# Kernel optimization log

Measured on AMD Instinct MI355X. Metric: run time of the kernel, lower is better.

The kernel has to match this reference:

```python
import jax, jax.numpy as jnp
import numpy as np

B, L, C, H = 32, 512, 512, 8
DH = C // H
LN_EPS = 1e-5


def setup_inputs() -> dict:
    key = jax.random.key(0)
    ks = jax.random.split(key, 5)
    x = jax.random.normal(ks[0], (B, L, C), dtype=jnp.float32)
    # nn.Linear weights are (out, in); y = x @ W.T
    wq = jax.random.normal(ks[1], (C, C), dtype=jnp.float32) * 0.02
    wk = jax.random.normal(ks[2], (C, C), dtype=jnp.float32) * 0.02
    wv = jax.random.normal(ks[3], (C, C), dtype=jnp.float32) * 0.02
    # source zero-inits the bias table; use small randoms so it actually contributes
    bias_table = jax.random.normal(ks[4], (2 * L - 1, H), dtype=jnp.float32) * 0.02
    gamma = jnp.ones((C,), dtype=jnp.float32)
    beta = jnp.zeros((C,), dtype=jnp.float32)
    coords = np.arange(L)
    rel_index = jnp.asarray(coords[None, :] - coords[:, None] + (L - 1), dtype=jnp.int32)  # (L, L)
    return {"x": x, "wq": wq, "wk": wk, "wv": wv, "bias_table": bias_table,
            "gamma": gamma, "beta": beta, "rel_index": rel_index}


def reference(x, wq, wk, wv, bias_table, gamma, beta, rel_index):
    Bx, Lx, Cx = x.shape
    scale = Cx ** (-0.5)  # note: scale uses full emb_size, as in source
    q = (x @ wq.T).reshape(Bx, Lx, H, DH).transpose(0, 2, 1, 3)  # (B,H,L,Dh)
    k = (x @ wk.T).reshape(Bx, Lx, H, DH).transpose(0, 2, 1, 3)
    v = (x @ wv.T).reshape(Bx, Lx, H, DH).transpose(0, 2, 1, 3)
    attn = jax.nn.softmax(jnp.einsum('bhqd,bhkd->bhqk', q, k) * scale, axis=-1)
    # post-softmax relative bias gather-add
    rel_bias = bias_table[rel_index]                # (L, L, H)
    attn = attn + rel_bias.transpose(2, 0, 1)[None]  # (1,H,L,L) broadcast
    out = jnp.einsum('bhqk,bhkd->bhqd', attn, v)
    out = out.transpose(0, 2, 1, 3).reshape(Bx, Lx, Cx)
    mu = out.mean(axis=-1, keepdims=True)
    var = jnp.mean(jnp.square(out - mu), axis=-1, keepdims=True)
    return gamma * (out - mu) * jax.lax.rsqrt(var + LN_EPS) + beta
```

## Files before the change

kernel.cpp:

```cpp
#include <hip/hip_runtime.h>
#include <hip/hip_bf16.h>

typedef unsigned short u16;
typedef __attribute__((ext_vector_type(8))) __bf16 bf16x8;
typedef __attribute__((ext_vector_type(4))) float f32x4;
typedef __attribute__((ext_vector_type(4))) unsigned int u32x4;

#define BB 32
#define LL 512
#define CC 512
#define HH 8
#define DH 64
#define MROWS (BB * LL)
#define NQKV  (3 * CC)

#define XB_BYTES ((size_t)MROWS * CC * 2)
#define WC_BYTES ((size_t)NQKV * CC * 2)
#define QKV_OFF  (XB_BYTES + WC_BYTES)

#define SCALE2 (0.044194173824159216f * 1.4426950408889634f)

#if __has_builtin(__builtin_amdgcn_exp2f)
#define EXP2(x) __builtin_amdgcn_exp2f(x)
#else
#define EXP2(x) exp2f(x)
#endif
#if __has_builtin(__builtin_amdgcn_rcpf)
#define RCP(x) __builtin_amdgcn_rcpf(x)
#else
#define RCP(x) (1.0f / (x))
#endif

__device__ inline u16 f2b(float f) {
  union { float f; unsigned u; } a; a.f = f;
  unsigned u = a.u;
  return (u16)((u + 0x7FFFu + ((u >> 16) & 1u)) >> 16);
}

__device__ inline unsigned pack2(float a, float b) {
  float2 f; f.x = a; f.y = b;
  union { __hip_bfloat162 h; unsigned u; } c;
  c.h = __float22bfloat162_rn(f);
  return c.u;
}

__global__ __launch_bounds__(256) void cvt_x(const float* __restrict__ x, u16* __restrict__ xb) {
  int i = blockIdx.x * 256 + threadIdx.x;
  float4 v = ((const float4*)x)[i];
  uint2 o; o.x = pack2(v.x, v.y); o.y = pack2(v.z, v.w);
  ((uint2*)xb)[i] = o;
}

__global__ __launch_bounds__(256) void cvt_w(const float* __restrict__ wq, const float* __restrict__ wk,
                                             const float* __restrict__ wv, u16* __restrict__ wcat) {
  int i = blockIdx.x * 256 + threadIdx.x;
  int e = i * 4;
  int n = e >> 9;
  int k = e & 511;
  const float* src = (n < 512) ? (wq + (size_t)n * 512)
                   : (n < 1024) ? (wk + (size_t)(n - 512) * 512)
                                : (wv + (size_t)(n - 1024) * 512);
  const float sc = (n < 512) ? SCALE2 : 1.0f;
  float4 v = *(const float4*)(src + k);
  uint2 o; o.x = pack2(v.x * sc, v.y * sc); o.y = pack2(v.z * sc, v.w * sc);
  *(uint2*)(wcat + (size_t)n * 512 + k) = o;
}

typedef __attribute__((address_space(1))) void* as1_void_p;
typedef __attribute__((address_space(3))) void* as3_void_p;

__device__ inline void async16(const u16* g, u16* l) {
#if __has_builtin(__builtin_amdgcn_global_load_lds)
  __builtin_amdgcn_global_load_lds((as1_void_p)g, (as3_void_p)l, 16, 0, 0);
#else
  *(uint4*)l = *(const uint4*)g;
#endif
}

__global__ __launch_bounds__(256) void gemm_qkv(const u16* __restrict__ A, const u16* __restrict__ Bw,
                                                u16* __restrict__ Cm) {
  __shared__ u16 a_lds[128 * 32];
  __shared__ u16 b_lds[128 * 32];
  const int n0 = blockIdx.x * 128, m0 = blockIdx.y * 128;
  const int t = threadIdx.x, l = t & 63;
  const int wrow = ((t >> 7) & 1) * 64, wcol = ((t >> 6) & 1) * 64;
  const int lr = l & 15, lq = l >> 4;

  f32x4 acc[4][4] = {};

  for (int k0 = 0; k0 < 512; k0 += 32) {
    {
      int c0 = t, c1 = t + 256;
      async16(A  + (size_t)(m0 + (c0 >> 2)) * 512 + k0 + (c0 & 3) * 8, &a_lds[c0 * 8]);
      async16(A  + (size_t)(m0 + (c1 >> 2)) * 512 + k0 + (c1 & 3) * 8, &a_lds[c1 * 8]);
      async16(Bw + (size_t)(n0 + (c0 >> 2)) * 512 + k0 + (c0 & 3) * 8, &b_lds[c0 * 8]);
      async16(Bw + (size_t)(n0 + (c1 >> 2)) * 512 + k0 + (c1 & 3) * 8, &b_lds[c1 * 8]);
    }
    __syncthreads();
    bf16x8 af[4], bfr[4];
#pragma unroll
    for (int r = 0; r < 4; ++r) af[r]  = *(const bf16x8*)&a_lds[(wrow + r * 16 + lr) * 32 + lq * 8];
#pragma unroll
    for (int c = 0; c < 4; ++c) bfr[c] = *(const bf16x8*)&b_lds[(wcol + c * 16 + lr) * 32 + lq * 8];
#pragma unroll
    for (int r = 0; r < 4; ++r)
#pragma unroll
      for (int c = 0; c < 4; ++c)
        acc[r][c] = __builtin_amdgcn_mfma_f32_16x16x32_bf16(af[r], bfr[c], acc[r][c], 0, 0, 0);
    __syncthreads();
  }
#pragma unroll
  for (int r = 0; r < 4; ++r) {
#pragma unroll
    for (int i = 0; i < 4; ++i) {
      int m = m0 + wrow + r * 16 + lq * 4 + i;
      u16* crow = Cm + (size_t)m * NQKV + n0 + wcol;
#pragma unroll
      for (int c = 0; c < 4; ++c)
        crow[c * 16 + lr] = f2b(acc[r][c][i]);
    }
  }
}

__global__ __launch_bounds__(256) void transpose_v(const u16* __restrict__ qkv, u16* __restrict__ vT,
                                                   const float* __restrict__ bias_table,
                                                   float* __restrict__ biasT) {
  if (blockIdx.y == 4) {
    if (blockIdx.x < 32) {
      int i = blockIdx.x * 256 + threadIdx.x;
      if (i < 1023 * 8) {
        float v = bias_table[i];
        int rel = i >> 3, hh = i & 7;
        biasT[hh * 1024 + rel] = v;
      }
    }
    return;
  }
  const int bh = blockIdx.x;
  const int b = bh >> 3, h = bh & 7;
  const int lc0 = blockIdx.y * 128;
  __shared__ u16 tile[32 * 72];
  const int t = threadIdx.x;
  for (int lc = lc0; lc < lc0 + 128; lc += 32) {
    int lrow = t >> 3, dcol = (t & 7) * 8;
    const u16* src = qkv + (size_t)(b * 512 + lc + lrow) * NQKV + 1024 + h * 64 + dcol;
    *(uint4*)&tile[lrow * 72 + dcol] = *(const uint4*)src;
    __syncthreads();
    int d = t >> 2, lp = (t & 3) * 8;
    union { ushort4 v4[2]; u16 s[8]; } tmp;
#pragma unroll
    for (int j = 0; j < 8; ++j) tmp.s[j] = tile[(lp + j) * 72 + d];
    *(uint4*)&vT[(size_t)(bh * 64 + d) * 512 + lc + lp] = *(uint4*)&tmp;
    __syncthreads();
  }
}

__global__ __launch_bounds__(256, 4) void attn_kernel(const u16* __restrict__ qkv, const u16* __restrict__ vT,
                                                      const float* __restrict__ biasT,
                                                      float* __restrict__ out) {
  __shared__ u16 p_lds[32 * 512];
  __shared__ float bias_lds[544];
  __shared__ float reds[4][32];

  const int flat = blockIdx.x;
  const int bh = ((flat >> 7) << 3) | (flat & 7);
  const int q0 = ((flat >> 3) & 15) * 32;
  const int b = bh >> 3, h = bh & 7;
  const int t = threadIdx.x, l = t & 63, w = t >> 6;
  const int lr = l & 15, lq = l >> 4;

  {
    const int rel0 = 480 - q0;
    const float* bsrc = biasT + h * 1024 + rel0;
    for (int i = t; i < 543; i += 256)
      bias_lds[i] = bsrc[i];
  }
  asm volatile("s_waitcnt vmcnt(0)" ::: "memory");

  bf16x8 bq[2][2];
#pragma unroll
  for (int qt = 0; qt < 2; ++qt) {
    const u16* qrow = qkv + (size_t)(b * 512 + q0 + qt * 16 + lr) * NQKV + h * 64;
    bq[qt][0] = *(const bf16x8*)(qrow + lq * 8);
    bq[qt][1] = *(const bf16x8*)(qrow + 32 + lq * 8);
  }

  const u16* kbase = qkv + (size_t)(b * 512 + w * 128 + lr) * NQKV + 512 + h * 64 + lq * 8;
  u32x4 akr[4][2];
  f32x4 sT[2][8];

#define KISSUE(slot, ct) { const u16* kr = kbase + (size_t)(ct) * 16 * NQKV;   \
    asm volatile("global_load_dwordx4 %0, %2, off\n\t"                         \
                 "global_load_dwordx4 %1, %2, off offset:64"                   \
                 : "=&v"(akr[slot][0]), "=&v"(akr[slot][1]) : "v"(kr)); }
#define KSTEP(ct, lit, doissue) {                                              \
    if (doissue) KISSUE(((ct) + 3) & 3, (ct) + 3)                              \
    asm volatile("s_waitcnt vmcnt(" lit ")"                                    \
                 : "+v"(akr[(ct) & 3][0]), "+v"(akr[(ct) & 3][1]));            \
    bf16x8 ak0 = __builtin_bit_cast(bf16x8, akr[(ct) & 3][0]);                 \
    bf16x8 ak1 = __builtin_bit_cast(bf16x8, akr[(ct) & 3][1]);                 \
    f32x4 a0 = {0.f, 0.f, 0.f, 0.f}, a1 = {0.f, 0.f, 0.f, 0.f};                \
    a0 = __builtin_amdgcn_mfma_f32_16x16x32_bf16(ak0, bq[0][0], a0, 0, 0, 0);  \
    a0 = __builtin_amdgcn_mfma_f32_16x16x32_bf16(ak1, bq[0][1], a0, 0, 0, 0);  \
    a1 = __builtin_amdgcn_mfma_f32_16x16x32_bf16(ak0, bq[1][0], a1, 0, 0, 0);  \
    a1 = __builtin_amdgcn_mfma_f32_16x16x32_bf16(ak1, bq[1][1], a1, 0, 0, 0);  \
    sT[0][ct] = a0; sT[1][ct] = a1; }

  KISSUE(0, 0) KISSUE(1, 1) KISSUE(2, 2)
  KSTEP(0, "6", 1) KSTEP(1, "6", 1) KSTEP(2, "6", 1) KSTEP(3, "6", 1)
  KSTEP(4, "6", 1) KSTEP(5, "4", 0) KSTEP(6, "2", 0) KSTEP(7, "0", 0)
#undef KSTEP
#undef KISSUE

  float sq[2];
#pragma unroll
  for (int qt = 0; qt < 2; ++qt) {
    float s0 = 0.f, s1 = 0.f, s2 = 0.f, s3 = 0.f;
#pragma unroll
    for (int ct = 0; ct < 8; ++ct) {
      float e0 = EXP2(sT[qt][ct][0]);
      float e1 = EXP2(sT[qt][ct][1]);
      float e2 = EXP2(sT[qt][ct][2]);
      float e3 = EXP2(sT[qt][ct][3]);
      sT[qt][ct][0] = e0; sT[qt][ct][1] = e1;
      sT[qt][ct][2] = e2; sT[qt][ct][3] = e3;
      s0 += e0; s1 += e1; s2 += e2; s3 += e3;
    }
    sq[qt] = (s0 + s1) + (s2 + s3);
  }
  {
    float t0 = sq[0], t1 = sq[1];
    float u0 = __shfl_xor(t0, 16, 64), u1 = __shfl_xor(t1, 16, 64);
    t0 += u0; t1 += u1;
    u0 = __shfl_xor(t0, 32, 64); u1 = __shfl_xor(t1, 32, 64);
    sq[0] = t0 + u0; sq[1] = t1 + u1;
  }
  if (lq == 0) { reds[w][lr] = sq[0]; reds[w][16 + lr] = sq[1]; }

  asm volatile("s_waitcnt lgkmcnt(0)" ::: "memory");
  __builtin_amdgcn_s_barrier();
  asm volatile("" ::: "memory");

  float rinv[2];
#pragma unroll
  for (int qt = 0; qt < 2; ++qt)
    rinv[qt] = RCP(reds[0][qt * 16 + lr] + reds[1][qt * 16 + lr] +
                   reds[2][qt * 16 + lr] + reds[3][qt * 16 + lr]);

  const u16* vrow = vT + (size_t)(bh * 64 + w * 16 + lr) * 512 + lq * 8;
  u32x4 avr[8];
#define VISSUE(slot, olit)                                                     \
  asm volatile("global_load_dwordx4 %0, %1, off offset:" olit                  \
               : "=&v"(avr[slot]) : "v"(vrow));
  VISSUE(0, "0")   VISSUE(1, "64")  VISSUE(2, "128") VISSUE(3, "192")
  VISSUE(4, "256") VISSUE(5, "320") VISSUE(6, "384") VISSUE(7, "448")

#define PACK_QT(qt)                                                            \
  {                                                                            \
    const int qlocal = (qt) * 16 + lr;                                         \
    u16* prow = p_lds + qlocal * 512;                                          \
    const int boff = w * 128 + lq * 4 + 31 - qlocal;                           \
    _Pragma("unroll")                                                          \
    for (int ct = 0; ct < 8; ++ct) {                                           \
      const int gsw = w * 8 + (ct ^ (lr & 7));                                 \
      float p0 = sT[qt][ct][0] * rinv[qt] + bias_lds[boff + ct * 16 + 0];      \
      float p1 = sT[qt][ct][1] * rinv[qt] + bias_lds[boff + ct * 16 + 1];      \
      float p2 = sT[qt][ct][2] * rinv[qt] + bias_lds[boff + ct * 16 + 2];      \
      float p3 = sT[qt][ct][3] * rinv[qt] + bias_lds[boff + ct * 16 + 3];      \
      uint2 pk; pk.x = pack2(p0, p1); pk.y = pack2(p2, p3);                    \
      *(uint2*)&prow[gsw * 16 + lq * 4] = pk;                                  \
    }                                                                          \
  }
  PACK_QT(0)
  PACK_QT(1)
#undef PACK_QT

  asm volatile("s_waitcnt lgkmcnt(0)" ::: "memory");
  __builtin_amdgcn_s_barrier();
  asm volatile("" ::: "memory");

  f32x4 accP[2] = {};
  bf16x8 bp[2][2];
#define LDP(kb, qt) \
  (*(const bf16x8*)&p_lds[((qt) * 16 + lr) * 512 + \
    (((2 * (kb) + (lq >> 1)) & ~7) | (((2 * (kb) + (lq >> 1)) & 7) ^ (lr & 7))) * 16 + (lq & 1) * 8])
  bp[0][0] = LDP(0, 0);
  bp[0][1] = LDP(0, 1);
#define PVSTEP(kb, lit, doissue, olit) {                                       \
    asm volatile("s_waitcnt vmcnt(" lit ")" : "+v"(avr[(kb) & 7]));            \
    if ((kb) < 15) {                                                           \
      bp[((kb) + 1) & 1][0] = LDP((kb) + 1, 0);                                \
      bp[((kb) + 1) & 1][1] = LDP((kb) + 1, 1);                                \
    }                                                                          \
    bf16x8 av = __builtin_bit_cast(bf16x8, avr[(kb) & 7]);                     \
    accP[0] = __builtin_amdgcn_mfma_f32_16x16x32_bf16(av, bp[(kb) & 1][0], accP[0], 0, 0, 0); \
    accP[1] = __builtin_amdgcn_mfma_f32_16x16x32_bf16(av, bp[(kb) & 1][1], accP[1], 0, 0, 0); \
    if (doissue) VISSUE((kb) & 7, olit) }
  PVSTEP(0,  "7", 1, "512") PVSTEP(1,  "7", 1, "576")
  PVSTEP(2,  "7", 1, "640") PVSTEP(3,  "7", 1, "704")
  PVSTEP(4,  "7", 1, "768") PVSTEP(5,  "7", 1, "832")
  PVSTEP(6,  "7", 1, "896") PVSTEP(7,  "7", 1, "960")
  PVSTEP(8,  "7", 0, "0")   PVSTEP(9,  "6", 0, "0")
  PVSTEP(10, "5", 0, "0")   PVSTEP(11, "4", 0, "0")
  PVSTEP(12, "3", 0, "0")   PVSTEP(13, "2", 0, "0")
  PVSTEP(14, "1", 0, "0")   PVSTEP(15, "0", 0, "0")
#undef PVSTEP
#undef VISSUE
#undef LDP
#pragma unroll
  for (int qt = 0; qt < 2; ++qt)
    *(f32x4*)&out[(size_t)(b * 512 + q0 + qt * 16 + lr) * 512 + h * 64 + w * 16 + lq * 4] = accP[qt];
}

__global__ __launch_bounds__(256) void ln_kernel(float* __restrict__ out,
                                                 const float* __restrict__ gamma,
                                                 const float* __restrict__ beta) {
  const int t = threadIdx.x;
  const int r2 = t >> 7;
  const int row = blockIdx.x * 2 + r2;
  const int c = (t & 127) * 4;
  float* p = out + (size_t)row * 512;
  float4 v = *(float4*)(p + c);
  float s = v.x + v.y + v.z + v.w;
  float s2 = v.x * v.x + v.y * v.y + v.z * v.z + v.w * v.w;
#pragma unroll
  for (int d = 1; d < 64; d <<= 1) { s += __shfl_xor(s, d, 64); s2 += __shfl_xor(s2, d, 64); }
  __shared__ float ps[4], ps2[4];
  const int wv = t >> 6;
  if ((t & 63) == 0) { ps[wv] = s; ps2[wv] = s2; }
  __syncthreads();
  s  = ps[r2 * 2]  + ps[r2 * 2 + 1];
  s2 = ps2[r2 * 2] + ps2[r2 * 2 + 1];
  float mu = s * (1.0f / 512.0f);
  float var = s2 * (1.0f / 512.0f) - mu * mu;
  float rs = rsqrtf(var + 1e-5f);
  float4 g = *(const float4*)(gamma + c);
  float4 bb = *(const float4*)(beta + c);
  v.x = g.x * (v.x - mu) * rs + bb.x;
  v.y = g.y * (v.y - mu) * rs + bb.y;
  v.z = g.z * (v.z - mu) * rs + bb.z;
  v.w = g.w * (v.w - mu) * rs + bb.w;
  *(float4*)(p + c) = v;
}

extern "C" void kernel_launch(void* const* d_in, const int* in_sizes, int n_in,
                              void* d_out, int out_size, void* d_ws, size_t ws_size,
                              hipStream_t stream) {
  const float* x    = (const float*)d_in[0];
  const float* wq   = (const float*)d_in[1];
  const float* wk   = (const float*)d_in[2];
  const float* wv   = (const float*)d_in[3];
  const float* bias = (const float*)d_in[4];
  const float* gamma = (const float*)d_in[5];
  const float* beta  = (const float*)d_in[6];
  float* out = (float*)d_out;

  char* ws = (char*)d_ws;
  u16* xb   = (u16*)ws;
  u16* wcat = (u16*)(ws + XB_BYTES);
  u16* qkv  = (u16*)(ws + QKV_OFF);
  u16* vT   = xb;
  float* biasT = (float*)(ws + XB_BYTES);

  cvt_x<<<dim3((MROWS * CC) / 4 / 256), 256, 0, stream>>>(x, xb);
  cvt_w<<<dim3((NQKV * CC) / 4 / 256), 256, 0, stream>>>(wq, wk, wv, wcat);
  gemm_qkv<<<dim3(NQKV / 128, MROWS / 128), 256, 0, stream>>>(xb, wcat, qkv);
  transpose_v<<<dim3(256, 5), 256, 0, stream>>>(qkv, vT, bias, biasT);
  attn_kernel<<<dim3(16 * 256), 256, 0, stream>>>(qkv, vT, biasT, out);
  ln_kernel<<<dim3(MROWS / 2), 256, 0, stream>>>(out, gamma, beta);
}
```

Measured before the change: 224.3 us.

## Process four 32-row query tiles per attention block in a loop

Each attention block now loops over four consecutive 32-row query tiles, covering 128 query rows, and the grid shrinks from 4096 to 1024 blocks. The relative-bias slice is loaded into LDS once per block with a wider window, and the reduction buffer is double-buffered so consecutive iterations do not collide. The aim is to amortize per-block setup (bias load, launch, address calculation) over more work. In exchange, iterations within a block run serially, there are fewer blocks to hide latency across CUs, and K/V are still re-read for every tile.

```diff
diff --git a/kernel.cpp b/kernel.cpp
--- a/kernel.cpp
+++ b/kernel.cpp
@@ -159,35 +159,47 @@
                                                       const float* __restrict__ biasT,
                                                       float* __restrict__ out) {
   __shared__ u16 p_lds[32 * 512];
-  __shared__ float bias_lds[544];
-  __shared__ float reds[4][32];
+  __shared__ float bias_lds[640];
+  __shared__ float reds[2][4][32];
 
   const int flat = blockIdx.x;
-  const int bh = ((flat >> 7) << 3) | (flat & 7);
-  const int q0 = ((flat >> 3) & 15) * 32;
-  const int b = bh >> 3, h = bh & 7;
+  const int h = flat & 7;
+  const int qslot = (flat >> 3) & 3;
+  const int b = flat >> 5;
+  const int bh = b * 8 + h;
+  const int q0 = qslot * 128;
   const int t = threadIdx.x, l = t & 63, w = t >> 6;
   const int lr = l & 15, lq = l >> 4;
 
   {
-    const int rel0 = 480 - q0;
+    const int rel0 = 384 - q0;
     const float* bsrc = biasT + h * 1024 + rel0;
-    for (int i = t; i < 543; i += 256)
+    for (int i = t; i < 639; i += 256)
       bias_lds[i] = bsrc[i];
   }
   asm volatile("s_waitcnt vmcnt(0)" ::: "memory");
 
-  bf16x8 bq[2][2];
-#pragma unroll
-  for (int qt = 0; qt < 2; ++qt) {
-    const u16* qrow = qkv + (size_t)(b * 512 + q0 + qt * 16 + lr) * NQKV + h * 64;
-    bq[qt][0] = *(const bf16x8*)(qrow + lq * 8);
-    bq[qt][1] = *(const bf16x8*)(qrow + 32 + lq * 8);
-  }
-
   const u16* kbase = qkv + (size_t)(b * 512 + w * 128 + lr) * NQKV + 512 + h * 64 + lq * 8;
-  u32x4 akr[4][2];
-  f32x4 sT[2][8];
+  const u16* vrow  = vT  + (size_t)(bh * 64 + w * 16 + lr) * 512 + lq * 8;
+
+#pragma unroll 1
+  for (int j = 0; j < 4; ++j) {
+    const int q0j = q0 + j * 32;
+
+    u32x4 bqr[2][2];
+    {
+      const u16* q0r = qkv + (size_t)(b * 512 + q0j + lr) * NQKV + h * 64 + lq * 8;
+      const u16* q1r = q0r + (size_t)16 * NQKV;
+      asm volatile("global_load_dwordx4 %0, %2, off\n\t"
+                   "global_load_dwordx4 %1, %2, off offset:64"
+                   : "=&v"(bqr[0][0]), "=&v"(bqr[0][1]) : "v"(q0r));
+      asm volatile("global_load_dwordx4 %0, %2, off\n\t"
+                   "global_load_dwordx4 %1, %2, off offset:64"
+                   : "=&v"(bqr[1][0]), "=&v"(bqr[1][1]) : "v"(q1r));
+    }
+
+    u32x4 akr[4][2];
+    f32x4 sT[2][8];
 
 #define KISSUE(slot, ct) { const u16* kr = kbase + (size_t)(ct) * 16 * NQKV;   \
     asm volatile("global_load_dwordx4 %0, %2, off\n\t"                         \
@@ -200,92 +212,94 @@
     bf16x8 ak0 = __builtin_bit_cast(bf16x8, akr[(ct) & 3][0]);                 \
     bf16x8 ak1 = __builtin_bit_cast(bf16x8, akr[(ct) & 3][1]);                 \
     f32x4 a0 = {0.f, 0.f, 0.f, 0.f}, a1 = {0.f, 0.f, 0.f, 0.f};                \
-    a0 = __builtin_amdgcn_mfma_f32_16x16x32_bf16(ak0, bq[0][0], a0, 0, 0, 0);  \
-    a0 = __builtin_amdgcn_mfma_f32_16x16x32_bf16(ak1, bq[0][1], a0, 0, 0, 0);  \
-    a1 = __builtin_amdgcn_mfma_f32_16x16x32_bf16(ak0, bq[1][0], a1, 0, 0, 0);  \
-    a1 = __builtin_amdgcn_mfma_f32_16x16x32_bf16(ak1, bq[1][1], a1, 0, 0, 0);  \
+    a0 = __builtin_amdgcn_mfma_f32_16x16x32_bf16(ak0, __builtin_bit_cast(bf16x8, bqr[0][0]), a0, 0, 0, 0); \
+    a0 = __builtin_amdgcn_mfma_f32_16x16x32_bf16(ak1, __builtin_bit_cast(bf16x8, bqr[0][1]), a0, 0, 0, 0); \
+    a1 = __builtin_amdgcn_mfma_f32_16x16x32_bf16(ak0, __builtin_bit_cast(bf16x8, bqr[1][0]), a1, 0, 0, 0); \
+    a1 = __builtin_amdgcn_mfma_f32_16x16x32_bf16(ak1, __builtin_bit_cast(bf16x8, bqr[1][1]), a1, 0, 0, 0); \
     sT[0][ct] = a0; sT[1][ct] = a1; }
 
-  KISSUE(0, 0) KISSUE(1, 1) KISSUE(2, 2)
-  KSTEP(0, "6", 1) KSTEP(1, "6", 1) KSTEP(2, "6", 1) KSTEP(3, "6", 1)
-  KSTEP(4, "6", 1) KSTEP(5, "4", 0) KSTEP(6, "2", 0) KSTEP(7, "0", 0)
+    KISSUE(0, 0) KISSUE(1, 1) KISSUE(2, 2)
+    asm volatile("s_waitcnt vmcnt(6)"
+                 : "+v"(bqr[0][0]), "+v"(bqr[0][1]), "+v"(bqr[1][0]), "+v"(bqr[1][1]));
+    KSTEP(0, "6", 1) KSTEP(1, "6", 1) KSTEP(2, "6", 1) KSTEP(3, "6", 1)
+    KSTEP(4, "6", 1) KSTEP(5, "4", 0) KSTEP(6, "2", 0) KSTEP(7, "0", 0)
 #undef KSTEP
 #undef KISSUE
 
-  float sq[2];
-#pragma unroll
-  for (int qt = 0; qt < 2; ++qt) {
-    float s0 = 0.f, s1 = 0.f, s2 = 0.f, s3 = 0.f;
-#pragma unroll
-    for (int ct = 0; ct < 8; ++ct) {
-      float e0 = EXP2(sT[qt][ct][0]);
-      float e1 = EXP2(sT[qt][ct][1]);
-      float e2 = EXP2(sT[qt][ct][2]);
-      float e3 = EXP2(sT[qt][ct][3]);
-      sT[qt][ct][0] = e0; sT[qt][ct][1] = e1;
-      sT[qt][ct][2] = e2; sT[qt][ct][3] = e3;
-      s0 += e0; s1 += e1; s2 += e2; s3 += e3;
-    }
-    sq[qt] = (s0 + s1) + (s2 + s3);
-  }
-  {
-    float t0 = sq[0], t1 = sq[1];
-    float u0 = __shfl_xor(t0, 16, 64), u1 = __shfl_xor(t1, 16, 64);
-    t0 += u0; t1 += u1;
-    u0 = __shfl_xor(t0, 32, 64); u1 = __shfl_xor(t1, 32, 64);
-    sq[0] = t0 + u0; sq[1] = t1 + u1;
-  }
-  if (lq == 0) { reds[w][lr] = sq[0]; reds[w][16 + lr] = sq[1]; }
-
-  asm volatile("s_waitcnt lgkmcnt(0)" ::: "memory");
-  __builtin_amdgcn_s_barrier();
-  asm volatile("" ::: "memory");
-
-  float rinv[2];
-#pragma unroll
-  for (int qt = 0; qt < 2; ++qt)
-    rinv[qt] = RCP(reds[0][qt * 16 + lr] + reds[1][qt * 16 + lr] +
-                   reds[2][qt * 16 + lr] + reds[3][qt * 16 + lr]);
-
-  const u16* vrow = vT + (size_t)(bh * 64 + w * 16 + lr) * 512 + lq * 8;
-  u32x4 avr[8];
+    float sq[2];
+#pragma unroll
+    for (int qt = 0; qt < 2; ++qt) {
+      float s0 = 0.f, s1 = 0.f, s2 = 0.f, s3 = 0.f;
+#pragma unroll
+      for (int ct = 0; ct < 8; ++ct) {
+        float e0 = EXP2(sT[qt][ct][0]);
+        float e1 = EXP2(sT[qt][ct][1]);
+        float e2 = EXP2(sT[qt][ct][2]);
+        float e3 = EXP2(sT[qt][ct][3]);
+        sT[qt][ct][0] = e0; sT[qt][ct][1] = e1;
+        sT[qt][ct][2] = e2; sT[qt][ct][3] = e3;
+        s0 += e0; s1 += e1; s2 += e2; s3 += e3;
+      }
+      sq[qt] = (s0 + s1) + (s2 + s3);
+    }
+    {
+      float t0 = sq[0], t1 = sq[1];
+      float u0 = __shfl_xor(t0, 16, 64), u1 = __shfl_xor(t1, 16, 64);
+      t0 += u0; t1 += u1;
+      u0 = __shfl_xor(t0, 32, 64); u1 = __shfl_xor(t1, 32, 64);
+      sq[0] = t0 + u0; sq[1] = t1 + u1;
+    }
+    float (*rd)[32] = reds[j & 1];
+    if (lq == 0) { rd[w][lr] = sq[0]; rd[w][16 + lr] = sq[1]; }
+
+    asm volatile("s_waitcnt lgkmcnt(0)" ::: "memory");
+    __builtin_amdgcn_s_barrier();
+    asm volatile("" ::: "memory");
+
+    float rinv[2];
+#pragma unroll
+    for (int qt = 0; qt < 2; ++qt)
+      rinv[qt] = RCP(rd[0][qt * 16 + lr] + rd[1][qt * 16 + lr] +
+                     rd[2][qt * 16 + lr] + rd[3][qt * 16 + lr]);
+
+    u32x4 avr[8];
 #define VISSUE(slot, olit)                                                     \
-  asm volatile("global_load_dwordx4 %0, %1, off offset:" olit                  \
-               : "=&v"(avr[slot]) : "v"(vrow));
-  VISSUE(0, "0")   VISSUE(1, "64")  VISSUE(2, "128") VISSUE(3, "192")
-  VISSUE(4, "256") VISSUE(5, "320") VISSUE(6, "384") VISSUE(7, "448")
+    asm volatile("global_load_dwordx4 %0, %1, off offset:" olit                \
+                 : "=&v"(avr[slot]) : "v"(vrow));
+    VISSUE(0, "0")   VISSUE(1, "64")  VISSUE(2, "128") VISSUE(3, "192")
+    VISSUE(4, "256") VISSUE(5, "320") VISSUE(6, "384") VISSUE(7, "448")
 
 #define PACK_QT(qt)                                                            \
-  {                                                                            \
-    const int qlocal = (qt) * 16 + lr;                                         \
-    u16* prow = p_lds + qlocal * 512;                                          \
-    const int boff = w * 128 + lq * 4 + 31 - qlocal;                           \
-    _Pragma("unroll")                                                          \
-    for (int ct = 0; ct < 8; ++ct) {                                           \
-      const int gsw = w * 8 + (ct ^ (lr & 7));                                 \
-      float p0 = sT[qt][ct][0] * rinv[qt] + bias_lds[boff + ct * 16 + 0];      \
-      float p1 = sT[qt][ct][1] * rinv[qt] + bias_lds[boff + ct * 16 + 1];      \
-      float p2 = sT[qt][ct][2] * rinv[qt] + bias_lds[boff + ct * 16 + 2];      \
-      float p3 = sT[qt][ct][3] * rinv[qt] + bias_lds[boff + ct * 16 + 3];      \
-      uint2 pk; pk.x = pack2(p0, p1); pk.y = pack2(p2, p3);                    \
-      *(uint2*)&prow[gsw * 16 + lq * 4] = pk;                                  \
-    }                                                                          \
-  }
-  PACK_QT(0)
-  PACK_QT(1)
+    {                                                                          \
+      const int qlocal = (qt) * 16 + lr;                                       \
+      u16* prow = p_lds + qlocal * 512;                                        \
+      const int boff = w * 128 + lq * 4 + 127 - 32 * j - qlocal;               \
+      _Pragma("unroll")                                                        \
+      for (int ct = 0; ct < 8; ++ct) {                                         \
+        const int gsw = w * 8 + (ct ^ (lr & 7));                               \
+        float p0 = sT[qt][ct][0] * rinv[qt] + bias_lds[boff + ct * 16 + 0];    \
+        float p1 = sT[qt][ct][1] * rinv[qt] + bias_lds[boff + ct * 16 + 1];    \
+        float p2 = sT[qt][ct][2] * rinv[qt] + bias_lds[boff + ct * 16 + 2];    \
+        float p3 = sT[qt][ct][3] * rinv[qt] + bias_lds[boff + ct * 16 + 3];    \
+        uint2 pk; pk.x = pack2(p0, p1); pk.y = pack2(p2, p3);                  \
+        *(uint2*)&prow[gsw * 16 + lq * 4] = pk;                                \
+      }                                                                        \
+    }
+    PACK_QT(0)
+    PACK_QT(1)
 #undef PACK_QT
 
-  asm volatile("s_waitcnt lgkmcnt(0)" ::: "memory");
-  __builtin_amdgcn_s_barrier();
-  asm volatile("" ::: "memory");
-
-  f32x4 accP[2] = {};
-  bf16x8 bp[2][2];
+    asm volatile("s_waitcnt lgkmcnt(0)" ::: "memory");
+    __builtin_amdgcn_s_barrier();
+    asm volatile("" ::: "memory");
+
+    f32x4 accP[2] = {};
+    bf16x8 bp[2][2];
 #define LDP(kb, qt) \
-  (*(const bf16x8*)&p_lds[((qt) * 16 + lr) * 512 + \
-    (((2 * (kb) + (lq >> 1)) & ~7) | (((2 * (kb) + (lq >> 1)) & 7) ^ (lr & 7))) * 16 + (lq & 1) * 8])
-  bp[0][0] = LDP(0, 0);
-  bp[0][1] = LDP(0, 1);
+    (*(const bf16x8*)&p_lds[((qt) * 16 + lr) * 512 + \
+      (((2 * (kb) + (lq >> 1)) & ~7) | (((2 * (kb) + (lq >> 1)) & 7) ^ (lr & 7))) * 16 + (lq & 1) * 8])
+    bp[0][0] = LDP(0, 0);
+    bp[0][1] = LDP(0, 1);
 #define PVSTEP(kb, lit, doissue, olit) {                                       \
     asm volatile("s_waitcnt vmcnt(" lit ")" : "+v"(avr[(kb) & 7]));            \
     if ((kb) < 15) {                                                           \
@@ -296,20 +310,21 @@
     accP[0] = __builtin_amdgcn_mfma_f32_16x16x32_bf16(av, bp[(kb) & 1][0], accP[0], 0, 0, 0); \
     accP[1] = __builtin_amdgcn_mfma_f32_16x16x32_bf16(av, bp[(kb) & 1][1], accP[1], 0, 0, 0); \
     if (doissue) VISSUE((kb) & 7, olit) }
-  PVSTEP(0,  "7", 1, "512") PVSTEP(1,  "7", 1, "576")
-  PVSTEP(2,  "7", 1, "640") PVSTEP(3,  "7", 1, "704")
-  PVSTEP(4,  "7", 1, "768") PVSTEP(5,  "7", 1, "832")
-  PVSTEP(6,  "7", 1, "896") PVSTEP(7,  "7", 1, "960")
-  PVSTEP(8,  "7", 0, "0")   PVSTEP(9,  "6", 0, "0")
-  PVSTEP(10, "5", 0, "0")   PVSTEP(11, "4", 0, "0")
-  PVSTEP(12, "3", 0, "0")   PVSTEP(13, "2", 0, "0")
-  PVSTEP(14, "1", 0, "0")   PVSTEP(15, "0", 0, "0")
+    PVSTEP(0,  "7", 1, "512") PVSTEP(1,  "7", 1, "576")
+    PVSTEP(2,  "7", 1, "640") PVSTEP(3,  "7", 1, "704")
+    PVSTEP(4,  "7", 1, "768") PVSTEP(5,  "7", 1, "832")
+    PVSTEP(6,  "7", 1, "896") PVSTEP(7,  "7", 1, "960")
+    PVSTEP(8,  "7", 0, "0")   PVSTEP(9,  "6", 0, "0")
+    PVSTEP(10, "5", 0, "0")   PVSTEP(11, "4", 0, "0")
+    PVSTEP(12, "3", 0, "0")   PVSTEP(13, "2", 0, "0")
+    PVSTEP(14, "1", 0, "0")   PVSTEP(15, "0", 0, "0")
 #undef PVSTEP
 #undef VISSUE
 #undef LDP
 #pragma unroll
-  for (int qt = 0; qt < 2; ++qt)
-    *(f32x4*)&out[(size_t)(b * 512 + q0 + qt * 16 + lr) * 512 + h * 64 + w * 16 + lq * 4] = accP[qt];
+    for (int qt = 0; qt < 2; ++qt)
+      *(f32x4*)&out[(size_t)(b * 512 + q0j + qt * 16 + lr) * 512 + h * 64 + w * 16 + lq * 4] = accP[qt];
+  }
 }
 
 __global__ __launch_bounds__(256) void ln_kernel(float* __restrict__ out,
@@ -366,6 +381,6 @@
   cvt_w<<<dim3((NQKV * CC) / 4 / 256), 256, 0, stream>>>(wq, wk, wv, wcat);
   gemm_qkv<<<dim3(NQKV / 128, MROWS / 128), 256, 0, stream>>>(xb, wcat, qkv);
   transpose_v<<<dim3(256, 5), 256, 0, stream>>>(qkv, vT, bias, biasT);
-  attn_kernel<<<dim3(16 * 256), 256, 0, stream>>>(qkv, vT, biasT, out);
+  attn_kernel<<<dim3(1024), 256, 0, stream>>>(qkv, vT, biasT, out);
   ln_kernel<<<dim3(MROWS / 2), 256, 0, stream>>>(out, gamma, beta);
 }
```

Measured after the change: 238.4 us. 6.3% more time.
